# Performance work log

Measured on AMD Instinct MI355X. Metric: run time of the kernel, lower is better.

## Reference

```python
import jax, jax.numpy as jnp
import numpy as np

B, T_IN, T_OUT, N, C, H, K1 = 4, 12, 24, 5000, 32, 8, 17  # K1 = k+1 (self included)
SIGMA_RATIO = 2.0
BETA = 0.8  # Swish beta
W_THRESH = 1e-5


def setup_inputs() -> dict:
    key = jax.random.key(0)
    k1, k2, k3, k4, k5 = jax.random.split(key, 5)
    x = jax.random.normal(k1, (B, T_IN, N, C), jnp.float32)
    nearest_nodes = jax.random.randint(k2, (N, K1), 0, N)  # int indices; -1 allowed by module semantics
    nearest_dists = jax.random.uniform(k3, (N, K1), jnp.float32) * 100.0
    W_shrink = jax.random.normal(k4, (T_IN * H, T_OUT - T_IN), jnp.float32) / np.float32(np.sqrt(T_IN * H))
    b_shrink = jax.random.normal(k5, (T_OUT - T_IN,), jnp.float32) * 0.01
    return {"x": x, "nearest_nodes": nearest_nodes, "nearest_dists": nearest_dists,
            "W_shrink": W_shrink, "b_shrink": b_shrink}


def reference(x, nearest_nodes, nearest_dists, W_shrink, b_shrink):
    Bx, t, n, c = x.shape
    sigma = nearest_dists.max() / SIGMA_RATIO
    lam = jnp.arange(1, H + 1, dtype=jnp.float32) / H  # (H,)
    nd = nearest_dists.reshape(-1)                      # (N*K1,)
    nn = nearest_nodes.reshape(-1)                      # (N*K1,)
    # GCN weights: exp(-d^2 * lambda / sigma^2), zeroed for missing (-1) neighbors and tiny values
    w = jnp.exp(-(nd[:, None] ** 2) * lam / (sigma ** 2))  # (N*K1, H)
    w = jnp.where(nn[:, None] == -1, 0.0, w)
    w = jnp.where(w < W_THRESH, 0.0, w)
    # pad row so index -1 hits zeros (jax -1 wraps to last row, matching torch)
    pad_x = jnp.concatenate([x, jnp.zeros((Bx, t, 1, c), x.dtype)], axis=2)
    x_nb = pad_x[:, :, nn].reshape(Bx, t, n, K1, c)         # gathered neighbors (B,t,N,K1,C)
    w3 = w.reshape(n, K1, H)
    # fused gather-weight-sum over neighbor dim j -> (B,t,N,H,C)
    agg = jnp.einsum('btnjc,njh->btnhc', x_nb, w3)
    # (B,t,N,H,C) -> (B,N,C,t,H) -> (B,N,C,t*H)
    feat = agg.transpose(0, 2, 4, 1, 3).reshape(Bx, n, c, t * H)
    y = feat @ W_shrink + b_shrink                          # (B,N,C,T-t_in)
    y = y.transpose(0, 3, 1, 2)                             # (B,T-t_in,N,C)
    y = y * jax.nn.sigmoid(BETA * y)                        # Swish
    return jnp.concatenate([x, y], axis=1)                  # (B,T,N,C)
```

## Files before the change

### kernel.cpp

```cpp
#include <hip/hip_runtime.h>

#define BB     4
#define T_IN   12
#define T_OUT  24
#define NNODES 5000
#define CC     32
#define HH     8
#define K1     17
#define O_OUT  12
#define XSTRIDE (NNODES*CC)
#define TPU     (NNODES*16)

#define XB2_BN  192
#define XB2_B   (NNODES*XB2_BN)
#define JP      9
#define VJPD    36
#define VQD     (JP*VJPD)
#define VND     (4*VQD)

__global__ void max_reduce_kernel(const float* __restrict__ d, int n,
                                  unsigned* __restrict__ out) {
    float m = 0.0f;
    for (int i = blockIdx.x * blockDim.x + threadIdx.x; i < n;
         i += gridDim.x * blockDim.x)
        m = fmaxf(m, d[i]);
#pragma unroll
    for (int off = 32; off > 0; off >>= 1)
        m = fmaxf(m, __shfl_down(m, off, 64));
    if ((threadIdx.x & 63) == 0)
        atomicMax(out, __float_as_uint(m));
}

__device__ inline unsigned bf16rne(float f) {
    unsigned u = __float_as_uint(f);
    return (u + 0x7FFFu + ((u >> 16) & 1u)) >> 16;
}

__global__ void prep5_kernel(const float4* __restrict__ x,
                             float4* __restrict__ out,
                             uint4* __restrict__ xb2,
                             const float* __restrict__ nd,
                             unsigned* __restrict__ maxbits) {
    const int gs = gridDim.x * blockDim.x;
    const int g0 = blockIdx.x * blockDim.x + threadIdx.x;

    {
        float m = 0.0f;
        for (int i = g0; i < NNODES * K1; i += gs) m = fmaxf(m, nd[i]);
#pragma unroll
        for (int off = 32; off > 0; off >>= 1)
            m = fmaxf(m, __shfl_down(m, off, 64));
        if ((threadIdx.x & 63) == 0 && m > 0.0f)
            atomicMax(maxbits, __float_as_uint(m));
    }

    const int totalA = BB * T_IN * NNODES;
    for (int i = g0; i < totalA; i += gs) {
        int bt = i / NNODES;
        int nd_ = i - bt * NNODES;
        int b  = bt / T_IN;
        int t  = bt - b * T_IN;
        const float4* xr = x + (size_t)i * 8;
        float4* orow = out + ((size_t)(b * T_OUT + t) * NNODES + nd_) * 8;
        uint4* xrow  = xb2 + ((size_t)(b * NNODES + nd_) * T_IN + t) * 4;
#pragma unroll
        for (int vq = 0; vq < 4; ++vq) {
            float4 v0 = xr[2 * vq], v1 = xr[2 * vq + 1];
            orow[2 * vq] = v0; orow[2 * vq + 1] = v1;
            uint4 pk;
            pk.x = bf16rne(v0.x) | (bf16rne(v0.y) << 16);
            pk.y = bf16rne(v0.z) | (bf16rne(v0.w) << 16);
            pk.z = bf16rne(v1.x) | (bf16rne(v1.y) << 16);
            pk.w = bf16rne(v1.z) | (bf16rne(v1.w) << 16);
            xrow[vq] = pk;
        }
    }
}

struct VBlk { uint4 v[9]; };

__device__ __forceinline__ unsigned u4c(const uint4& u, int i) {
    switch (i) { case 0: return u.x; case 1: return u.y;
                 case 2: return u.z; default: return u.w; }
}

#define DOT2(ACC, XP, VP) \
    asm("v_dot2_f32_bf16 %0, %1, %2, %0" : "+v"(ACC) : "v"(XP), "v"(VP))

__launch_bounds__(256)
__global__ void gnn_main9_kernel(const unsigned* __restrict__ xb2,
                                 const float* __restrict__ nd,
                                 const float* __restrict__ Wsh,
                                 const int* __restrict__ nn,
                                 const float* __restrict__ bsh,
                                 const unsigned* __restrict__ maxbits,
                                 float* __restrict__ out) {
    __shared__ float pb2[2][24][65];
    __shared__ unsigned Vl[VND];
    __shared__ float wjl[144];
    __shared__ float bl[O_OUT];

    const int n    = blockIdx.x;
    const int tid  = threadIdx.x;
    const int q    = __builtin_amdgcn_readfirstlane(tid >> 6);
    const int lane = tid & 63;
    const int bb   = lane >> 4;
    const int c2   = lane & 15;

    if (tid < O_OUT) bl[tid] = bsh[tid];

    int nnv[18];
#pragma unroll
    for (int j = 0; j < K1; ++j) nnv[j] = max(nn[n * K1 + j], 0);
    nnv[17] = nnv[16];

    const unsigned* xlane = xb2 + bb * XB2_B + 48 * q + c2;

#define XLOADP(E0, E1, E2, O0, O1, O2, JPI) do {                             \
        const unsigned* xe_ = xlane + nnv[2 * (JPI)] * XB2_BN;               \
        const unsigned* xo_ = xlane + nnv[2 * (JPI) + 1] * XB2_BN;           \
        E0 = xe_[0]; E1 = xe_[16]; E2 = xe_[32];                             \
        O0 = xo_[0]; O1 = xo_[16]; O2 = xo_[32];                             \
    } while (0)

    unsigned e00, e01, e02, o00, o01, o02;
    unsigned e10, e11, e12, o10, o11, o12;
    unsigned e20, e21, e22, o20, o21, o22;

    XLOADP(e00, e01, e02, o00, o01, o02, 0);
    XLOADP(e10, e11, e12, o10, o11, o12, 1);

    const int t14 = tid / 12;
    const int o14 = tid - t14 * 12;
    float Wcol[8];
    if (tid < 144) {
#pragma unroll
        for (int h = 0; h < 8; ++h) Wcol[h] = Wsh[(t14 * 8 + h) * 12 + o14];
        int j = tid >> 3, h = tid & 7;
        float wv = 0.f;
        if (j < K1) {
            float mx = __uint_as_float(*maxbits);
            float inv_s2 = 4.0f / (mx * mx);
            float dv = nd[n * K1 + j];
            float lam = (float)(h + 1) * 0.125f;
            wv = expf(-dv * dv * lam * inv_s2);
            if (nn[n * K1 + j] == -1 || wv < 1e-5f) wv = 0.0f;
        }
        wjl[tid] = wv;
    }
    __syncthreads();

    if (tid < 144) {
        const int vi = (t14 / 3) * VQD + (t14 % 3) * 12 + o14;
#pragma unroll
        for (int jp = 0; jp < JP; ++jp) {
            float4 a0 = *(const float4*)&wjl[jp * 16];
            float4 a1 = *(const float4*)&wjl[jp * 16 + 4];
            float4 b0 = *(const float4*)&wjl[jp * 16 + 8];
            float4 b1 = *(const float4*)&wjl[jp * 16 + 12];
            float wa[8] = {a0.x, a0.y, a0.z, a0.w, a1.x, a1.y, a1.z, a1.w};
            float wb[8] = {b0.x, b0.y, b0.z, b0.w, b1.x, b1.y, b1.z, b1.w};
            float v0 = 0.f, v1 = 0.f;
#pragma unroll
            for (int h = 0; h < 8; ++h) {
                v0 = fmaf(wa[h], Wcol[h], v0);
                v1 = fmaf(wb[h], Wcol[h], v1);
            }
            Vl[vi + jp * VJPD] = bf16rne(v0) | (bf16rne(v1) << 16);
        }
    }

    float pf[24];
#pragma unroll
    for (int i = 0; i < 24; ++i) pf[i] = 0.f;

    __syncthreads();

#define VLOADP(DST, JPI) do {                                                \
        const uint4* vp_ = (const uint4*)&Vl[q * VQD + (JPI) * VJPD];        \
        _Pragma("unroll")                                                    \
        for (int i_ = 0; i_ < 9; ++i_) DST.v[i_] = vp_[i_];                  \
    } while (0)

#define COMPP(VV, E0, E1, E2, O0, O1, O2) do {                               \
        unsigned xe_[3] = {E0, E1, E2};                                      \
        unsigned xo_[3] = {O0, O1, O2};                                      \
        _Pragma("unroll")                                                    \
        for (int t_ = 0; t_ < 3; ++t_) {                                     \
            unsigned plo_ = __builtin_amdgcn_perm(xe_[t_], xo_[t_],          \
                                                  0x01000504u);              \
            unsigned phi_ = __builtin_amdgcn_perm(xe_[t_], xo_[t_],          \
                                                  0x03020706u);              \
            _Pragma("unroll")                                                \
            for (int o_ = 0; o_ < 12; ++o_) {                                \
                unsigned vp_ = u4c(VV.v[t_ * 3 + (o_ >> 2)], o_ & 3);        \
                DOT2(pf[o_],      plo_, vp_);                                \
                DOT2(pf[12 + o_], phi_, vp_);                                \
            }                                                                \
        }                                                                    \
    } while (0)

    VBlk va, vb;
    VLOADP(va, 0);
    VLOADP(vb, 1);
    XLOADP(e20, e21, e22, o20, o21, o22, 2);
    COMPP(va, e00, e01, e02, o00, o01, o02);
    VLOADP(va, 2);
    XLOADP(e00, e01, e02, o00, o01, o02, 3);
    COMPP(vb, e10, e11, e12, o10, o11, o12);
    VLOADP(vb, 3);
    XLOADP(e10, e11, e12, o10, o11, o12, 4);
    COMPP(va, e20, e21, e22, o20, o21, o22);
    VLOADP(va, 4);
    XLOADP(e20, e21, e22, o20, o21, o22, 5);
    COMPP(vb, e00, e01, e02, o00, o01, o02);
    VLOADP(vb, 5);
    XLOADP(e00, e01, e02, o00, o01, o02, 6);
    COMPP(va, e10, e11, e12, o10, o11, o12);
    VLOADP(va, 6);
    XLOADP(e10, e11, e12, o10, o11, o12, 7);
    COMPP(vb, e20, e21, e22, o20, o21, o22);
    VLOADP(vb, 7);
    XLOADP(e20, e21, e22, o20, o21, o22, 8);
    COMPP(va, e00, e01, e02, o00, o01, o02);
    VLOADP(va, 8);
    COMPP(vb, e10, e11, e12, o10, o11, o12);
    COMPP(va, e20, e21, e22, o20, o21, o22);

#undef VLOADP
#undef XLOADP
#undef COMPP

    if (q >= 2) {
#pragma unroll
        for (int i = 0; i < 24; ++i) pb2[q - 2][i][lane] = pf[i];
    }
    __syncthreads();
    if (q < 2) {
#pragma unroll
        for (int i = 0; i < 24; ++i) pf[i] += pb2[q][i][lane];
    }
    if (q == 1) {
#pragma unroll
        for (int i = 0; i < 24; ++i) pb2[1][i][lane] = pf[i];
    }
    __syncthreads();
    if (q == 0) {
        float* ob = out + ((size_t)(bb * T_OUT + T_IN) * NNODES + n) * CC + 2 * c2;
#pragma unroll
        for (int o = 0; o < O_OUT; ++o) {
            float v0 = pf[o]      + pb2[1][o][lane]      + bl[o];
            float v1 = pf[12 + o] + pb2[1][12 + o][lane] + bl[o];
            float s0 = v0 / (1.f + expf(-0.8f * v0));
            float s1 = v1 / (1.f + expf(-0.8f * v1));
            *(float2*)(ob + (size_t)o * XSTRIDE) = make_float2(s0, s1);
        }
    }
}

template <int PACK>
__global__ void prep_kernel(const float4* __restrict__ x,
                            float4* __restrict__ out,
                            uint2* __restrict__ xb) {
    const int PLANE4 = NNODES * CC / 4;
    const int total  = BB * T_IN * PLANE4;
    for (int i = blockIdx.x * blockDim.x + threadIdx.x; i < total;
         i += gridDim.x * blockDim.x) {
        int bt = i / PLANE4;
        int qq = i - bt * PLANE4;
        int b  = bt / T_IN;
        int t  = bt - b * T_IN;
        float4 v = x[i];
        out[((size_t)(b * T_OUT + t)) * PLANE4 + qq] = v;
        if (PACK) {
            uint2 pk;
            pk.x = bf16rne(v.x) | (bf16rne(v.y) << 16);
            pk.y = bf16rne(v.z) | (bf16rne(v.w) << 16);
            xb[i] = pk;
        }
    }
}

template <int USEBF>
__launch_bounds__(256)
__global__ void gnn_main_kernel(const float* __restrict__ x,
                                const unsigned* __restrict__ xbu,
                                const int* __restrict__ nn,
                                const float* __restrict__ nd,
                                const float* __restrict__ Wsh,
                                const float* __restrict__ bsh,
                                const unsigned* __restrict__ maxbits,
                                float* __restrict__ out) {
    __shared__ float wl[K1][HH];
    __shared__ float Wl[96][O_OUT];
    __shared__ float bl_s[O_OUT];
    __shared__ int   nnl[K1];

    const int n   = blockIdx.x;
    const int tid = threadIdx.x;
    const int rg  = tid >> 4;
    const int c2  = tid & 15;
    const int b   = rg >> 2;
    const int q   = rg & 3;

    for (int i = tid; i < 288; i += 256)
        ((float4*)Wl)[i] = ((const float4*)Wsh)[i];
    if (tid < O_OUT) bl_s[tid] = bsh[tid];
    if (tid < K1 * HH) {
        int j = tid >> 3, h = tid & 7;
        int v = nn[n * K1 + j];
        float dv = nd[n * K1 + j];
        float mx = __uint_as_float(*maxbits);
        float inv_s2 = 4.0f / (mx * mx);
        float lam = (float)(h + 1) * 0.125f;
        float wv = expf(-dv * dv * lam * inv_s2);
        if (v == -1 || wv < 1e-5f) wv = 0.0f;
        wl[j][h] = wv;
    }
    if (tid < K1) nnl[tid] = max(nn[n * K1 + tid], 0);
    __syncthreads();

    float acc[3][2][8];
#pragma unroll
    for (int k = 0; k < 3; ++k)
#pragma unroll
        for (int cc = 0; cc < 2; ++cc)
#pragma unroll
            for (int h = 0; h < 8; ++h) acc[k][cc][h] = 0.f;

    if (USEBF) {
        const unsigned* xbase = xbu + (b * T_IN + 3 * q) * TPU + c2;
        unsigned ua0, ua1, ua2, ub0, ub1, ub2;
#define LOADB(u0, u1, u2, J) do {                                            \
        int idx_ = __builtin_amdgcn_readfirstlane(nnl[(J)]);                 \
        const unsigned* bp_ = xbase + idx_ * 16;                             \
        u0 = bp_[0]; u1 = bp_[TPU]; u2 = bp_[2 * TPU];                       \
    } while (0)
#define COMPB(u0, u1, u2, J) do {                                            \
        float4 wA_ = *(const float4*)&wl[(J)][0];                            \
        float4 wB_ = *(const float4*)&wl[(J)][4];                            \
        float wv_[8] = {wA_.x, wA_.y, wA_.z, wA_.w,                          \
                        wB_.x, wB_.y, wB_.z, wB_.w};                         \
        float xl_[3] = {__uint_as_float(u0 << 16),                           \
                        __uint_as_float(u1 << 16),                           \
                        __uint_as_float(u2 << 16)};                          \
        float xh_[3] = {__uint_as_float(u0 & 0xffff0000u),                   \
                        __uint_as_float(u1 & 0xffff0000u),                   \
                        __uint_as_float(u2 & 0xffff0000u)};                  \
        _Pragma("unroll")                                                    \
        for (int k_ = 0; k_ < 3; ++k_)                                       \
            _Pragma("unroll")                                                \
            for (int h_ = 0; h_ < 8; ++h_) {                                 \
                acc[k_][0][h_] = fmaf(wv_[h_], xl_[k_], acc[k_][0][h_]);     \
                acc[k_][1][h_] = fmaf(wv_[h_], xh_[k_], acc[k_][1][h_]);     \
            }                                                                \
    } while (0)
        LOADB(ua0, ua1, ua2, 0);
#pragma unroll 1
        for (int jj = 0; jj < 8; ++jj) {
            LOADB(ub0, ub1, ub2, 2 * jj + 1);
            COMPB(ua0, ua1, ua2, 2 * jj);
            LOADB(ua0, ua1, ua2, 2 * jj + 2);
            COMPB(ub0, ub1, ub2, 2 * jj + 1);
        }
        COMPB(ua0, ua1, ua2, 16);
#undef LOADB
#undef COMPB
    } else {
        const float* xbase = x + (b * T_IN + 3 * q) * XSTRIDE + 2 * c2;
        float2 xa0, xa1, xa2, xb0, xb1, xb2;
#define LOADJ(v0, v1, v2, J) do {                                            \
        int idx_ = __builtin_amdgcn_readfirstlane(nnl[(J)]);                 \
        const float* bp_ = xbase + idx_ * CC;                                \
        v0 = *(const float2*)(bp_);                                          \
        v1 = *(const float2*)(bp_ + XSTRIDE);                                \
        v2 = *(const float2*)(bp_ + 2 * XSTRIDE);                            \
    } while (0)
#define COMPJ(v0, v1, v2, J) do {                                            \
        float4 wA_ = *(const float4*)&wl[(J)][0];                            \
        float4 wB_ = *(const float4*)&wl[(J)][4];                            \
        float wv_[8] = {wA_.x, wA_.y, wA_.z, wA_.w,                          \
                        wB_.x, wB_.y, wB_.z, wB_.w};                         \
        float xv_[3][2] = {{v0.x, v0.y}, {v1.x, v1.y}, {v2.x, v2.y}};        \
        _Pragma("unroll")                                                    \
        for (int k_ = 0; k_ < 3; ++k_)                                       \
            _Pragma("unroll")                                                \
            for (int cc_ = 0; cc_ < 2; ++cc_)                                \
                _Pragma("unroll")                                            \
                for (int h_ = 0; h_ < 8; ++h_)                               \
                    acc[k_][cc_][h_] =                                       \
                        fmaf(wv_[h_], xv_[k_][cc_], acc[k_][cc_][h_]);       \
    } while (0)
        LOADJ(xa0, xa1, xa2, 0);
#pragma unroll 1
        for (int jj = 0; jj < 8; ++jj) {
            LOADJ(xb0, xb1, xb2, 2 * jj + 1);
            COMPJ(xa0, xa1, xa2, 2 * jj);
            LOADJ(xa0, xa1, xa2, 2 * jj + 2);
            COMPJ(xb0, xb1, xb2, 2 * jj + 1);
        }
        COMPJ(xa0, xa1, xa2, 16);
#undef LOADJ
#undef COMPJ
    }

    float p[2][O_OUT];
#pragma unroll
    for (int o = 0; o < O_OUT; ++o) { p[0][o] = 0.f; p[1][o] = 0.f; }
#pragma unroll
    for (int k = 0; k < 3; ++k) {
#pragma unroll
        for (int h = 0; h < 8; ++h) {
            int row = (3 * q + k) * 8 + h;
            const float4* wr = (const float4*)&Wl[row][0];
            float4 w0 = wr[0], w1 = wr[1], w2 = wr[2];
            float wrow[12] = {w0.x, w0.y, w0.z, w0.w,
                              w1.x, w1.y, w1.z, w1.w,
                              w2.x, w2.y, w2.z, w2.w};
            float a0 = acc[k][0][h], a1 = acc[k][1][h];
#pragma unroll
            for (int o = 0; o < O_OUT; ++o) {
                p[0][o] = fmaf(a0, wrow[o], p[0][o]);
                p[1][o] = fmaf(a1, wrow[o], p[1][o]);
            }
        }
    }
#pragma unroll
    for (int cc = 0; cc < 2; ++cc)
#pragma unroll
        for (int o = 0; o < O_OUT; ++o) {
            float v = p[cc][o];
            v += __shfl_xor(v, 16, 64);
            v += __shfl_xor(v, 32, 64);
            p[cc][o] = v;
        }
    if (q == 0) {
        float* ob = out + ((size_t)(b * T_OUT + T_IN) * NNODES + n) * CC + 2 * c2;
#pragma unroll
        for (int o = 0; o < O_OUT; ++o) {
            float v0 = p[0][o] + bl_s[o];
            float v1 = p[1][o] + bl_s[o];
            float s0 = v0 / (1.f + expf(-0.8f * v0));
            float s1 = v1 / (1.f + expf(-0.8f * v1));
            *(float2*)(ob + (size_t)o * XSTRIDE) = make_float2(s0, s1);
        }
    }
}

extern "C" void kernel_launch(void* const* d_in, const int* in_sizes, int n_in,
                              void* d_out, int out_size, void* d_ws, size_t ws_size,
                              hipStream_t stream) {
    const float* x   = (const float*)d_in[0];
    const int*   nn  = (const int*)d_in[1];
    const float* nd  = (const float*)d_in[2];
    const float* Wsh = (const float*)d_in[3];
    const float* bsh = (const float*)d_in[4];
    float* out = (float*)d_out;

    unsigned* maxbits = (unsigned*)d_ws;
    hipMemsetAsync(d_ws, 0, sizeof(unsigned), stream);

    const size_t xb2_off = 1024;
    const size_t xb2_sz  = (size_t)BB * NNODES * T_IN * 16 * 4;
    const size_t need2   = xb2_off + xb2_sz;

    if (ws_size >= need2) {
        uint4* xb2 = (uint4*)((char*)d_ws + xb2_off);

        prep5_kernel<<<2048, 256, 0, stream>>>(
            (const float4*)x, (float4*)out, xb2, nd, maxbits);
        gnn_main9_kernel<<<NNODES, 256, 0, stream>>>(
            (const unsigned*)xb2, nd, Wsh, nn, bsh, maxbits, out);
    } else {
        max_reduce_kernel<<<128, 256, 0, stream>>>(nd, NNODES * K1, maxbits);
        unsigned* xbu = (unsigned*)((char*)d_ws + 256);
        const size_t need1 = 256 + (size_t)BB * T_IN * NNODES * CC * 2;
        if (ws_size >= need1) {
            prep_kernel<1><<<2048, 256, 0, stream>>>((const float4*)x,
                                                     (float4*)out, (uint2*)xbu);
            gnn_main_kernel<1><<<NNODES, 256, 0, stream>>>(x, xbu, nn, nd, Wsh,
                                                           bsh, maxbits, out);
        } else {
            prep_kernel<0><<<2048, 256, 0, stream>>>((const float4*)x,
                                                     (float4*)out, (uint2*)xbu);
            gnn_main_kernel<0><<<NNODES, 256, 0, stream>>>(x, xbu, nn, nd, Wsh,
                                                           bsh, maxbits, out);
        }
    }
}
```

Before: 90.61 us.

## Split combined-weight build into separate kernel and map one node per wavefront

New measurement: 100.5 us. +10.9%, slower.

```diff
diff --git a/kernel.cpp b/kernel.cpp
--- a/kernel.cpp
+++ b/kernel.cpp
@@ -77,65 +77,15 @@
     }
 }
 
-struct VBlk { uint4 v[9]; };
-
-__device__ __forceinline__ unsigned u4c(const uint4& u, int i) {
-    switch (i) { case 0: return u.x; case 1: return u.y;
-                 case 2: return u.z; default: return u.w; }
-}
-
-#define DOT2(ACC, XP, VP) \
-    asm("v_dot2_f32_bf16 %0, %1, %2, %0" : "+v"(ACC) : "v"(XP), "v"(VP))
-
-__launch_bounds__(256)
-__global__ void gnn_main9_kernel(const unsigned* __restrict__ xb2,
-                                 const float* __restrict__ nd,
-                                 const float* __restrict__ Wsh,
-                                 const int* __restrict__ nn,
-                                 const float* __restrict__ bsh,
-                                 const unsigned* __restrict__ maxbits,
-                                 float* __restrict__ out) {
-    __shared__ float pb2[2][24][65];
-    __shared__ unsigned Vl[VND];
+__launch_bounds__(192)
+__global__ void vbuild4_kernel(const int* __restrict__ nn,
+                               const float* __restrict__ nd,
+                               const float* __restrict__ Wsh,
+                               const unsigned* __restrict__ maxbits,
+                               unsigned* __restrict__ Vb2) {
     __shared__ float wjl[144];
-    __shared__ float bl[O_OUT];
-
-    const int n    = blockIdx.x;
-    const int tid  = threadIdx.x;
-    const int q    = __builtin_amdgcn_readfirstlane(tid >> 6);
-    const int lane = tid & 63;
-    const int bb   = lane >> 4;
-    const int c2   = lane & 15;
-
-    if (tid < O_OUT) bl[tid] = bsh[tid];
-
-    int nnv[18];
-#pragma unroll
-    for (int j = 0; j < K1; ++j) nnv[j] = max(nn[n * K1 + j], 0);
-    nnv[17] = nnv[16];
-
-    const unsigned* xlane = xb2 + bb * XB2_B + 48 * q + c2;
-
-#define XLOADP(E0, E1, E2, O0, O1, O2, JPI) do {                             \
-        const unsigned* xe_ = xlane + nnv[2 * (JPI)] * XB2_BN;               \
-        const unsigned* xo_ = xlane + nnv[2 * (JPI) + 1] * XB2_BN;           \
-        E0 = xe_[0]; E1 = xe_[16]; E2 = xe_[32];                             \
-        O0 = xo_[0]; O1 = xo_[16]; O2 = xo_[32];                             \
-    } while (0)
-
-    unsigned e00, e01, e02, o00, o01, o02;
-    unsigned e10, e11, e12, o10, o11, o12;
-    unsigned e20, e21, e22, o20, o21, o22;
-
-    XLOADP(e00, e01, e02, o00, o01, o02, 0);
-    XLOADP(e10, e11, e12, o10, o11, o12, 1);
-
-    const int t14 = tid / 12;
-    const int o14 = tid - t14 * 12;
-    float Wcol[8];
+    const int n = blockIdx.x, tid = threadIdx.x;
     if (tid < 144) {
-#pragma unroll
-        for (int h = 0; h < 8; ++h) Wcol[h] = Wsh[(t14 * 8 + h) * 12 + o14];
         int j = tid >> 3, h = tid & 7;
         float wv = 0.f;
         if (j < K1) {
@@ -149,9 +99,13 @@
         wjl[tid] = wv;
     }
     __syncthreads();
-
     if (tid < 144) {
-        const int vi = (t14 / 3) * VQD + (t14 % 3) * 12 + o14;
+        const int t = tid / 12;
+        const int o = tid - t * 12;
+        float Wcol[8];
+#pragma unroll
+        for (int h = 0; h < 8; ++h) Wcol[h] = Wsh[(t * 8 + h) * 12 + o];
+        unsigned* vn = Vb2 + (size_t)n * VND + (t / 3) * VQD + (t % 3) * 12 + o;
 #pragma unroll
         for (int jp = 0; jp < JP; ++jp) {
             float4 a0 = *(const float4*)&wjl[jp * 16];
@@ -166,20 +120,57 @@
                 v0 = fmaf(wa[h], Wcol[h], v0);
                 v1 = fmaf(wb[h], Wcol[h], v1);
             }
-            Vl[vi + jp * VJPD] = bf16rne(v0) | (bf16rne(v1) << 16);
-        }
-    }
+            vn[jp * VJPD] = bf16rne(v0) | (bf16rne(v1) << 16);
+        }
+    }
+}
+
+struct VBlk { uint4 v[9]; };
+
+__device__ __forceinline__ unsigned u4c(const uint4& u, int i) {
+    switch (i) { case 0: return u.x; case 1: return u.y;
+                 case 2: return u.z; default: return u.w; }
+}
+
+#define DOT2(ACC, XP, VP) \
+    asm("v_dot2_f32_bf16 %0, %1, %2, %0" : "+v"(ACC) : "v"(XP), "s"(VP))
+
+__launch_bounds__(256)
+__global__ void gnn_main12_kernel(const unsigned* __restrict__ xb2,
+                                  const unsigned* __restrict__ Vb2,
+                                  const int* __restrict__ nn,
+                                  const float* __restrict__ bsh,
+                                  float* __restrict__ out) {
+    const int tid  = threadIdx.x;
+    const int w    = __builtin_amdgcn_readfirstlane(tid >> 6);
+    const int n    = blockIdx.x * 4 + w;
+    const int lane = tid & 63;
+    const int bb   = lane >> 4;
+    const int c2   = lane & 15;
+
+    int nnv[18];
+#pragma unroll
+    for (int j = 0; j < K1; ++j) nnv[j] = max(nn[n * K1 + j], 0);
+    nnv[17] = nnv[16];
+
+    const unsigned* xlane = xb2 + bb * XB2_B + c2;
+    const unsigned* vnode = Vb2 + (size_t)n * VND;
 
     float pf[24];
 #pragma unroll
     for (int i = 0; i < 24; ++i) pf[i] = 0.f;
 
-    __syncthreads();
-
-#define VLOADP(DST, JPI) do {                                                \
-        const uint4* vp_ = (const uint4*)&Vl[q * VQD + (JPI) * VJPD];        \
+#define VLOADP(DST, VB, JPI) do {                                            \
+        const uint4* vp_ = (const uint4*)((VB) + (JPI) * VJPD);              \
         _Pragma("unroll")                                                    \
         for (int i_ = 0; i_ < 9; ++i_) DST.v[i_] = vp_[i_];                  \
+    } while (0)
+
+#define XLOADP(E0, E1, E2, O0, O1, O2, XQ, JPI) do {                         \
+        const unsigned* xe_ = (XQ) + nnv[2 * (JPI)] * XB2_BN;                \
+        const unsigned* xo_ = (XQ) + nnv[2 * (JPI) + 1] * XB2_BN;            \
+        E0 = xe_[0]; E1 = xe_[16]; E2 = xe_[32];                             \
+        O0 = xo_[0]; O1 = xo_[16]; O2 = xo_[32];                             \
     } while (0)
 
 #define COMPP(VV, E0, E1, E2, O0, O1, O2) do {                               \
@@ -200,61 +191,58 @@
         }                                                                    \
     } while (0)
 
-    VBlk va, vb;
-    VLOADP(va, 0);
-    VLOADP(vb, 1);
-    XLOADP(e20, e21, e22, o20, o21, o22, 2);
-    COMPP(va, e00, e01, e02, o00, o01, o02);
-    VLOADP(va, 2);
-    XLOADP(e00, e01, e02, o00, o01, o02, 3);
-    COMPP(vb, e10, e11, e12, o10, o11, o12);
-    VLOADP(vb, 3);
-    XLOADP(e10, e11, e12, o10, o11, o12, 4);
-    COMPP(va, e20, e21, e22, o20, o21, o22);
-    VLOADP(va, 4);
-    XLOADP(e20, e21, e22, o20, o21, o22, 5);
-    COMPP(vb, e00, e01, e02, o00, o01, o02);
-    VLOADP(vb, 5);
-    XLOADP(e00, e01, e02, o00, o01, o02, 6);
-    COMPP(va, e10, e11, e12, o10, o11, o12);
-    VLOADP(va, 6);
-    XLOADP(e10, e11, e12, o10, o11, o12, 7);
-    COMPP(vb, e20, e21, e22, o20, o21, o22);
-    VLOADP(vb, 7);
-    XLOADP(e20, e21, e22, o20, o21, o22, 8);
-    COMPP(va, e00, e01, e02, o00, o01, o02);
-    VLOADP(va, 8);
-    COMPP(vb, e10, e11, e12, o10, o11, o12);
-    COMPP(va, e20, e21, e22, o20, o21, o22);
+#pragma unroll 1
+    for (int q = 0; q < 4; ++q) {
+        const unsigned* vbase = vnode + q * VQD;
+        const unsigned* xq    = xlane + 48 * q;
+
+        VBlk va, vb;
+        unsigned e00, e01, e02, o00, o01, o02;
+        unsigned e10, e11, e12, o10, o11, o12;
+        unsigned e20, e21, e22, o20, o21, o22;
+
+        XLOADP(e00, e01, e02, o00, o01, o02, xq, 0);
+        XLOADP(e10, e11, e12, o10, o11, o12, xq, 1);
+        VLOADP(va, vbase, 0);
+        VLOADP(vb, vbase, 1);
+        XLOADP(e20, e21, e22, o20, o21, o22, xq, 2);
+        COMPP(va, e00, e01, e02, o00, o01, o02);
+        VLOADP(va, vbase, 2);
+        XLOADP(e00, e01, e02, o00, o01, o02, xq, 3);
+        COMPP(vb, e10, e11, e12, o10, o11, o12);
+        VLOADP(vb, vbase, 3);
+        XLOADP(e10, e11, e12, o10, o11, o12, xq, 4);
+        COMPP(va, e20, e21, e22, o20, o21, o22);
+        VLOADP(va, vbase, 4);
+        XLOADP(e20, e21, e22, o20, o21, o22, xq, 5);
+        COMPP(vb, e00, e01, e02, o00, o01, o02);
+        VLOADP(vb, vbase, 5);
+        XLOADP(e00, e01, e02, o00, o01, o02, xq, 6);
+        COMPP(va, e10, e11, e12, o10, o11, o12);
+        VLOADP(va, vbase, 6);
+        XLOADP(e10, e11, e12, o10, o11, o12, xq, 7);
+        COMPP(vb, e20, e21, e22, o20, o21, o22);
+        VLOADP(vb, vbase, 7);
+        XLOADP(e20, e21, e22, o20, o21, o22, xq, 8);
+        COMPP(va, e00, e01, e02, o00, o01, o02);
+        VLOADP(va, vbase, 8);
+        COMPP(vb, e10, e11, e12, o10, o11, o12);
+        COMPP(va, e20, e21, e22, o20, o21, o22);
+    }
 
 #undef VLOADP
 #undef XLOADP
 #undef COMPP
 
-    if (q >= 2) {
-#pragma unroll
-        for (int i = 0; i < 24; ++i) pb2[q - 2][i][lane] = pf[i];
-    }
-    __syncthreads();
-    if (q < 2) {
-#pragma unroll
-        for (int i = 0; i < 24; ++i) pf[i] += pb2[q][i][lane];
-    }
-    if (q == 1) {
-#pragma unroll
-        for (int i = 0; i < 24; ++i) pb2[1][i][lane] = pf[i];
-    }
-    __syncthreads();
-    if (q == 0) {
-        float* ob = out + ((size_t)(bb * T_OUT + T_IN) * NNODES + n) * CC + 2 * c2;
-#pragma unroll
-        for (int o = 0; o < O_OUT; ++o) {
-            float v0 = pf[o]      + pb2[1][o][lane]      + bl[o];
-            float v1 = pf[12 + o] + pb2[1][12 + o][lane] + bl[o];
-            float s0 = v0 / (1.f + expf(-0.8f * v0));
-            float s1 = v1 / (1.f + expf(-0.8f * v1));
-            *(float2*)(ob + (size_t)o * XSTRIDE) = make_float2(s0, s1);
-        }
+    float* ob = out + ((size_t)(bb * T_OUT + T_IN) * NNODES + n) * CC + 2 * c2;
+#pragma unroll
+    for (int o = 0; o < O_OUT; ++o) {
+        float bo = bsh[o];
+        float v0 = pf[o] + bo;
+        float v1 = pf[12 + o] + bo;
+        float s0 = v0 / (1.f + expf(-0.8f * v0));
+        float s1 = v1 / (1.f + expf(-0.8f * v1));
+        *(float2*)(ob + (size_t)o * XSTRIDE) = make_float2(s0, s1);
     }
 }
 
@@ -462,15 +450,19 @@
 
     const size_t xb2_off = 1024;
     const size_t xb2_sz  = (size_t)BB * NNODES * T_IN * 16 * 4;
-    const size_t need2   = xb2_off + xb2_sz;
+    const size_t vb_off  = xb2_off + xb2_sz;
+    const size_t vb_sz   = (size_t)NNODES * VND * 4;
+    const size_t need2   = vb_off + vb_sz;
 
     if (ws_size >= need2) {
-        uint4* xb2 = (uint4*)((char*)d_ws + xb2_off);
+        uint4*    xb2 = (uint4*)((char*)d_ws + xb2_off);
+        unsigned* Vb2 = (unsigned*)((char*)d_ws + vb_off);
 
         prep5_kernel<<<2048, 256, 0, stream>>>(
             (const float4*)x, (float4*)out, xb2, nd, maxbits);
-        gnn_main9_kernel<<<NNODES, 256, 0, stream>>>(
-            (const unsigned*)xb2, nd, Wsh, nn, bsh, maxbits, out);
+        vbuild4_kernel<<<NNODES, 192, 0, stream>>>(nn, nd, Wsh, maxbits, Vb2);
+        gnn_main12_kernel<<<NNODES / 4, 256, 0, stream>>>(
+            (const unsigned*)xb2, Vb2, nn, bsh, out);
     } else {
         max_reduce_kernel<<<128, 256, 0, stream>>>(nd, NNODES * K1, maxbits);
         unsigned* xbu = (unsigned*)((char*)d_ws + 256);
```
